# Kernel tuning notes

Hardware: AMD Instinct MI355X
Metric: run time of the kernel (lower is better)

The kernel has to match this reference:

```python
import jax, jax.numpy as jnp
import numpy as np

B, S, D = 32, 2048, 1024
H = 8
D_ATTN = 256
D_HEAD = D_ATTN // H          # 32
D_HEAD_OUT = D // H           # 128
SOFTMAX_TEMP = 1.0


def setup_inputs() -> dict:
    key = jax.random.key(0)
    k0, k1, k2, k3, k4 = jax.random.split(key, 5)
    features = jax.random.normal(k0, (B, S, D), dtype=jnp.float32)
    # truncated-normal(std=0.01) init approximated with scaled normal
    w1 = jax.random.normal(k1, (H, D, D_HEAD), dtype=jnp.float32) * 0.01
    b1 = jax.random.normal(k2, (H, D_HEAD), dtype=jnp.float32) * 0.01
    w2 = jax.random.normal(k3, (H, D_HEAD, D_HEAD_OUT), dtype=jnp.float32) * 0.01
    b2 = jax.random.normal(k4, (H, D_HEAD_OUT), dtype=jnp.float32) * 0.01
    return {"features": features, "w1": w1, "b1": b1, "w2": w2, "b2": b2}


def reference(features, w1, b1, w2, b2):
    Bc, Sc, Dc = features.shape
    # per-head first projection: [B,H,S,d_head]
    h = jnp.einsum('bsd,hde->bhse', features, w1) + b1[None, :, None, :]
    h = jax.nn.gelu(h, approximate=False)  # torch nn.GELU default is exact erf
    # second projection: [B,H,S,d_head_out]
    logits = jnp.einsum('bhse,heo->bhso', h, w2) + b2[None, :, None, :]
    # softmax over seq dim (axis=2)
    smw = jax.nn.softmax(logits / SOFTMAX_TEMP, axis=2)
    # [B,H,S,D/H] -> [B,S,H,D/H] -> [B,S,D]
    smw = smw.transpose(0, 2, 1, 3).reshape(Bc, Sc, Dc)
    return (features * smw).sum(axis=1)  # [B,D]
```

## Files before the change

kernel.cpp:

```cpp
#include <hip/hip_runtime.h>
#include <hip/hip_bf16.h>
#include <math.h>

#define S_  2048
#define D_  1024

typedef __attribute__((ext_vector_type(8))) short short8;
typedef __attribute__((ext_vector_type(4))) float f32x4;

static __device__ __forceinline__ short f2bf(float x) {
    return __builtin_bit_cast(short, __float2bfloat16(x));
}
static __device__ __forceinline__ float bf2f(unsigned short s) {
    unsigned int u = ((unsigned int)s) << 16;
    return __builtin_bit_cast(float, u);
}

__device__ __forceinline__ void gl_lds16(const void* g, void* l) {
    __builtin_amdgcn_global_load_lds(
        (const __attribute__((address_space(1))) unsigned int*)g,
        (__attribute__((address_space(3))) unsigned int*)l, 16, 0, 0);
}

__global__ void prep_w1(const float* __restrict__ w1, short* __restrict__ w1p) {
    int tid = blockIdx.x * 256 + threadIdx.x;
    int lane = tid & 63;
    int fragid = tid >> 6;
    int cf = fragid & 15, ks = fragid >> 4;
    int col = cf * 16 + (lane & 15);
    int h = col >> 5, e = col & 31;
    int d0 = ks * 32 + (lane >> 4) * 8;
    short8 v;
#pragma unroll
    for (int r = 0; r < 8; ++r)
        v[r] = f2bf(w1[((size_t)h * D_ + (d0 + r)) * 32 + e]);
    *(short8*)(w1p + (size_t)tid * 8) = v;
}

__global__ void prep_w2(const float* __restrict__ w2, short* __restrict__ w2p) {
    int tid = blockIdx.x * 256 + threadIdx.x;
    int lane = tid & 63;
    int fragid = tid >> 6;
    int cf2 = fragid & 7, h = fragid >> 3;
    int o = cf2 * 16 + (lane & 15);
    int e0 = (lane >> 4) * 8;
    short8 v;
#pragma unroll
    for (int r = 0; r < 8; ++r)
        v[r] = f2bf(w2[((size_t)h * 32 + (e0 + r)) * 128 + o]);
    *(short8*)(w2p + (size_t)tid * 8) = v;
}

__global__ __launch_bounds__(256) void gemm1(
        const float* __restrict__ feat,
        const short* __restrict__ w1p,
        const float* __restrict__ b1,
        short* __restrict__ hact)
{
    __shared__ short hstage[4][32][136];

    const int tid = threadIdx.x;
    const int wv = tid >> 6;
    const int lane = tid & 63;
    const int lr = lane & 15;
    const int lg = lane >> 4;
    const int wr = wv >> 1, wc = wv & 1;
    const size_t m0 = (size_t)blockIdx.x * 64;

    const float* A0 = feat + (m0 + (size_t)(wr * 32 + lr)) * D_;
    const float* A1 = feat + (m0 + (size_t)(wr * 32 + 16 + lr)) * D_;
    const short8* Bp = (const short8*)w1p;

    const f32x4 vzero = {0.f, 0.f, 0.f, 0.f};
    f32x4 acc[2][8];
#pragma unroll
    for (int i = 0; i < 2; ++i)
#pragma unroll
        for (int j = 0; j < 8; ++j) acc[i][j] = vzero;

    f32x4 p0, p1, p2, p3;
    {
        const int o = lg * 8;
        p0 = *(const f32x4*)(A0 + o); p1 = *(const f32x4*)(A0 + o + 4);
        p2 = *(const f32x4*)(A1 + o); p3 = *(const f32x4*)(A1 + o + 4);
    }

    for (int ks = 0; ks < 32; ++ks) {
        short8 af0, af1;
        af0[0] = f2bf(p0.x); af0[1] = f2bf(p0.y); af0[2] = f2bf(p0.z); af0[3] = f2bf(p0.w);
        af0[4] = f2bf(p1.x); af0[5] = f2bf(p1.y); af0[6] = f2bf(p1.z); af0[7] = f2bf(p1.w);
        af1[0] = f2bf(p2.x); af1[1] = f2bf(p2.y); af1[2] = f2bf(p2.z); af1[3] = f2bf(p2.w);
        af1[4] = f2bf(p3.x); af1[5] = f2bf(p3.y); af1[6] = f2bf(p3.z); af1[7] = f2bf(p3.w);
        if (ks < 31) {
            const int o = (ks + 1) * 32 + lg * 8;
            p0 = *(const f32x4*)(A0 + o); p1 = *(const f32x4*)(A0 + o + 4);
            p2 = *(const f32x4*)(A1 + o); p3 = *(const f32x4*)(A1 + o + 4);
        }
        const short8* Bk = Bp + (size_t)ks * 1024 + (wc * 8) * 64 + lane;
#pragma unroll
        for (int j = 0; j < 8; ++j) {
            short8 b = Bk[j * 64];
            acc[0][j] = __builtin_amdgcn_mfma_f32_16x16x32_bf16(af0, b, acc[0][j], 0, 0, 0);
            acc[1][j] = __builtin_amdgcn_mfma_f32_16x16x32_bf16(af1, b, acc[1][j], 0, 0, 0);
        }
    }

#pragma unroll
    for (int cf = 0; cf < 8; ++cf) {
        const int col = wc * 128 + cf * 16 + lr;
        const float bias = b1[col];
#pragma unroll
        for (int a = 0; a < 2; ++a)
#pragma unroll
        for (int r = 0; r < 4; ++r) {
            const int row = a * 16 + lg * 4 + r;
            float x = acc[a][cf][r] + bias;
            float g = 0.5f * x * (1.0f + erff(x * 0.70710678118654752f));
            hstage[wv][row][cf * 16 + lr] = f2bf(g);
        }
    }
#pragma unroll
    for (int it = 0; it < 8; ++it) {
        const int idx = it * 64 + lane;
        const int row = idx >> 4;
        const int c8 = idx & 15;
        short8 v = *(const short8*)(&hstage[wv][row][c8 * 8]);
        *(short8*)(hact + (m0 + (size_t)(wr * 32 + row)) * 256 + wc * 128 + c8 * 8) = v;
    }
}

__global__ __launch_bounds__(256) void gemm2w(
        const short* __restrict__ hact,
        const float* __restrict__ feat,
        const short* __restrict__ w2p,
        const float* __restrict__ b2,
        float* __restrict__ pnum,
        float* __restrict__ pden)
{
    __shared__ __align__(16) char lds[41216];
    short* hstage = (short*)lds;
    unsigned short* Est = (unsigned short*)(lds + 8192);

    const int tid = threadIdx.x;
    const int wv = tid >> 6;
    const int lane = tid & 63;
    const int lr = lane & 15;
    const int lg = lane >> 4;
    const size_t m0 = (size_t)blockIdx.x * 16;

#pragma unroll
    for (int j = 0; j < 2; ++j)
        gl_lds16(hact + m0 * 256 + (size_t)(j * 256 + tid) * 8,
                 hstage + (j * 256 + wv * 64) * 8);

    float bias2[16];
#pragma unroll
    for (int cf = 0; cf < 16; ++cf)
        bias2[cf] = b2[(2 * wv + (cf >> 3)) * 128 + (cf & 7) * 16 + lr];

    __syncthreads();

    short8 ah0 = *(const short8*)(hstage + lr * 256 + (2 * wv + 0) * 32 + lg * 8);
    short8 ah1 = *(const short8*)(hstage + lr * 256 + (2 * wv + 1) * 32 + lg * 8);
    const f32x4 vzero = {0.f, 0.f, 0.f, 0.f};
#pragma unroll
    for (int cf = 0; cf < 16; ++cf) {
        const int h = 2 * wv + (cf >> 3);
        short8 bw = *(const short8*)(w2p + ((size_t)(h * 8 + (cf & 7)) * 64 + lane) * 8);
        f32x4 c = vzero;
        c = __builtin_amdgcn_mfma_f32_16x16x32_bf16((cf < 8) ? ah0 : ah1, bw, c, 0, 0, 0);
        const int colL = wv * 256 + (cf >> 3) * 128 + (cf & 7) * 16 + lr;
#pragma unroll
        for (int r = 0; r < 4; ++r) {
            float e = __expf(c[r] + bias2[cf]);
            Est[(lg * 4 + r) * 1032 + colL] = (unsigned short)f2bf(e);
        }
    }
    __syncthreads();

    const int c0 = tid * 4;
    f32x4 nacc = vzero, dacc = vzero;
    const float* fb = feat + m0 * D_ + c0;
#pragma unroll
    for (int row = 0; row < 16; ++row) {
        f32x4 fv = *(const f32x4*)(fb + (size_t)row * D_);
        unsigned long long ev = *(const unsigned long long*)(Est + row * 1032 + c0);
        f32x4 e;
        e.x = bf2f((unsigned short)(ev));
        e.y = bf2f((unsigned short)(ev >> 16));
        e.z = bf2f((unsigned short)(ev >> 32));
        e.w = bf2f((unsigned short)(ev >> 48));
        dacc += e;
        nacc += fv * e;
    }
    const size_t pb = (size_t)blockIdx.x * 1024 + c0;
    *(f32x4*)(pnum + pb) = nacc;
    *(f32x4*)(pden + pb) = dacc;
}

__global__ __launch_bounds__(256) void finalize3(
        const float* __restrict__ pnum,
        const float* __restrict__ pden,
        float* __restrict__ out)
{
    const int idx = blockIdx.x * 256 + threadIdx.x;
    const int b = idx >> 10;
    const int d = idx & 1023;
    const size_t base = (size_t)b * 128 * 1024 + d;
    float n = 0.f, dn = 0.f;
    for (int j = 0; j < 128; ++j) {
        n  += pnum[base + (size_t)j * 1024];
        dn += pden[base + (size_t)j * 1024];
    }
    out[idx] = n / dn;
}

extern "C" void kernel_launch(void* const* d_in, const int* in_sizes, int n_in,
                              void* d_out, int out_size, void* d_ws, size_t ws_size,
                              hipStream_t stream) {
    (void)in_sizes; (void)n_in; (void)out_size; (void)ws_size;
    const float* feat = (const float*)d_in[0];
    const float* w1   = (const float*)d_in[1];
    const float* b1   = (const float*)d_in[2];
    const float* w2   = (const float*)d_in[3];
    const float* b2   = (const float*)d_in[4];
    float* out = (float*)d_out;

    char* ws = (char*)d_ws;
    short* hact = (short*)ws;
    float* pnum = (float*)(ws + (32ull << 20));
    float* pden = (float*)(ws + (48ull << 20));
    short* w1p  = (short*)(ws + (64ull << 20));
    short* w2p  = (short*)(ws + (64ull << 20) + (512ull << 10));

    prep_w1<<<128, 256, 0, stream>>>(w1, w1p);
    prep_w2<<<16, 256, 0, stream>>>(w2, w2p);
    gemm1<<<1024, 256, 0, stream>>>(feat, w1p, b1, hact);
    gemm2w<<<4096, 256, 0, stream>>>(hact, feat, w2p, b2, pnum, pden);
    finalize3<<<128, 256, 0, stream>>>(pnum, pden, out);
}
```

Before: 217.2 us.

## Stage gemm1 operands through triple-buffered LDS with async global-to-LDS loads

gemm1 now uses 128-row by 128-column tiles, with each block covering half of the 256 output columns. Feature and packed W1 tiles are loaded straight into a 3-stage LDS ring with global_load_lds, using an XOR swizzle on the A tile to avoid bank conflicts. Previously A came from direct register prefetch and B from per-wave global reads. The goal is to overlap memory latency with MFMA work and let waves share B fragments through LDS. The cost is 72KB of LDS per block, which limits occupancy, and each feature row is now read by two blocks.

```diff
diff --git a/kernel.cpp b/kernel.cpp
--- a/kernel.cpp
+++ b/kernel.cpp
@@ -57,75 +57,125 @@
         const float* __restrict__ b1,
         short* __restrict__ hact)
 {
-    __shared__ short hstage[4][32][136];
+    __shared__ __align__(16) char lds[73728];
+    char* Abuf = lds;
+    char* Bbuf = lds + 49152;
+    short* hstage = (short*)lds;
 
     const int tid = threadIdx.x;
     const int wv = tid >> 6;
     const int lane = tid & 63;
     const int lr = lane & 15;
     const int lg = lane >> 4;
-    const int wr = wv >> 1, wc = wv & 1;
-    const size_t m0 = (size_t)blockIdx.x * 64;
-
-    const float* A0 = feat + (m0 + (size_t)(wr * 32 + lr)) * D_;
-    const float* A1 = feat + (m0 + (size_t)(wr * 32 + 16 + lr)) * D_;
-    const short8* Bp = (const short8*)w1p;
+    const int wr = wv >> 1, wc2 = wv & 1;
+    const int mblk = blockIdx.x >> 1, nblk = blockIdx.x & 1;
+    const size_t m0 = (size_t)mblk * 128;
+
+    const int segA = tid & 7;
+    const int rA = tid >> 3;
+    const int swbA = (segA * 16) ^ ((rA & 7) << 4);
+    const float* gA = feat + (m0 + rA) * D_ + (swbA >> 2);
+    const short* gB = w1p + (size_t)(nblk * 8) * 512 + tid * 8;
+
+    auto stageA = [&](int buf, int ks) {
+        const float* g = gA + ks * 32;
+        char* d = Abuf + buf * 16384 + tid * 16;
+#pragma unroll
+        for (int q = 0; q < 4; ++q)
+            gl_lds16(g + (size_t)q * 32 * D_, d + q * 4096);
+    };
+    auto stageB = [&](int buf, int ks) {
+        const short* g = gB + ks * 8192;
+        char* d = Bbuf + buf * 8192 + tid * 16;
+        gl_lds16(g, d);
+        gl_lds16(g + 2048, d + 4096);
+    };
 
     const f32x4 vzero = {0.f, 0.f, 0.f, 0.f};
-    f32x4 acc[2][8];
-#pragma unroll
-    for (int i = 0; i < 2; ++i)
-#pragma unroll
-        for (int j = 0; j < 8; ++j) acc[i][j] = vzero;
-
-    f32x4 p0, p1, p2, p3;
-    {
-        const int o = lg * 8;
-        p0 = *(const f32x4*)(A0 + o); p1 = *(const f32x4*)(A0 + o + 4);
-        p2 = *(const f32x4*)(A1 + o); p3 = *(const f32x4*)(A1 + o + 4);
-    }
-
-    for (int ks = 0; ks < 32; ++ks) {
-        short8 af0, af1;
-        af0[0] = f2bf(p0.x); af0[1] = f2bf(p0.y); af0[2] = f2bf(p0.z); af0[3] = f2bf(p0.w);
-        af0[4] = f2bf(p1.x); af0[5] = f2bf(p1.y); af0[6] = f2bf(p1.z); af0[7] = f2bf(p1.w);
-        af1[0] = f2bf(p2.x); af1[1] = f2bf(p2.y); af1[2] = f2bf(p2.z); af1[3] = f2bf(p2.w);
-        af1[4] = f2bf(p3.x); af1[5] = f2bf(p3.y); af1[6] = f2bf(p3.z); af1[7] = f2bf(p3.w);
-        if (ks < 31) {
-            const int o = (ks + 1) * 32 + lg * 8;
-            p0 = *(const f32x4*)(A0 + o); p1 = *(const f32x4*)(A0 + o + 4);
-            p2 = *(const f32x4*)(A1 + o); p3 = *(const f32x4*)(A1 + o + 4);
-        }
-        const short8* Bk = Bp + (size_t)ks * 1024 + (wc * 8) * 64 + lane;
-#pragma unroll
-        for (int j = 0; j < 8; ++j) {
-            short8 b = Bk[j * 64];
-            acc[0][j] = __builtin_amdgcn_mfma_f32_16x16x32_bf16(af0, b, acc[0][j], 0, 0, 0);
-            acc[1][j] = __builtin_amdgcn_mfma_f32_16x16x32_bf16(af1, b, acc[1][j], 0, 0, 0);
-        }
-    }
-
-#pragma unroll
-    for (int cf = 0; cf < 8; ++cf) {
-        const int col = wc * 128 + cf * 16 + lr;
-        const float bias = b1[col];
-#pragma unroll
-        for (int a = 0; a < 2; ++a)
-#pragma unroll
-        for (int r = 0; r < 4; ++r) {
-            const int row = a * 16 + lg * 4 + r;
-            float x = acc[a][cf][r] + bias;
-            float g = 0.5f * x * (1.0f + erff(x * 0.70710678118654752f));
-            hstage[wv][row][cf * 16 + lr] = f2bf(g);
-        }
-    }
-#pragma unroll
-    for (int it = 0; it < 8; ++it) {
-        const int idx = it * 64 + lane;
-        const int row = idx >> 4;
-        const int c8 = idx & 15;
-        short8 v = *(const short8*)(&hstage[wv][row][c8 * 8]);
-        *(short8*)(hact + (m0 + (size_t)(wr * 32 + row)) * 256 + wc * 128 + c8 * 8) = v;
+    f32x4 acc[4][4];
+#pragma unroll
+    for (int i = 0; i < 4; ++i)
+#pragma unroll
+        for (int j = 0; j < 4; ++j) acc[i][j] = vzero;
+
+    const int axor = (lr & 7) << 4;
+
+    auto compute = [&](int bi) {
+        const char* Ab = Abuf + bi * 16384;
+        const char* Bb = Bbuf + bi * 8192;
+        short8 bfr0 = *(const short8*)(Bb + ((wc2 * 4 + 0) * 64 + lane) * 16);
+        short8 bfr1 = *(const short8*)(Bb + ((wc2 * 4 + 1) * 64 + lane) * 16);
+        short8 bfr2 = *(const short8*)(Bb + ((wc2 * 4 + 2) * 64 + lane) * 16);
+        short8 bfr3 = *(const short8*)(Bb + ((wc2 * 4 + 3) * 64 + lane) * 16);
+#pragma unroll
+        for (int i = 0; i < 4; ++i) {
+            const int row = wr * 64 + i * 16 + lr;
+            f32x4 alo = *(const f32x4*)(Ab + row * 128 + ((lg * 32) ^ axor));
+            f32x4 ahi = *(const f32x4*)(Ab + row * 128 + ((lg * 32 + 16) ^ axor));
+            short8 af;
+            af[0] = f2bf(alo.x); af[1] = f2bf(alo.y);
+            af[2] = f2bf(alo.z); af[3] = f2bf(alo.w);
+            af[4] = f2bf(ahi.x); af[5] = f2bf(ahi.y);
+            af[6] = f2bf(ahi.z); af[7] = f2bf(ahi.w);
+            acc[i][0] = __builtin_amdgcn_mfma_f32_16x16x32_bf16(af, bfr0, acc[i][0], 0, 0, 0);
+            acc[i][1] = __builtin_amdgcn_mfma_f32_16x16x32_bf16(af, bfr1, acc[i][1], 0, 0, 0);
+            acc[i][2] = __builtin_amdgcn_mfma_f32_16x16x32_bf16(af, bfr2, acc[i][2], 0, 0, 0);
+            acc[i][3] = __builtin_amdgcn_mfma_f32_16x16x32_bf16(af, bfr3, acc[i][3], 0, 0, 0);
+        }
+    };
+
+    stageA(0, 0); stageB(0, 0);
+    stageA(1, 1); stageB(1, 1);
+
+    int cur = 0;
+    for (int ks = 0; ks < 30; ++ks) {
+        asm volatile("s_waitcnt vmcnt(6)" ::: "memory");
+        __builtin_amdgcn_sched_barrier(0);
+        __builtin_amdgcn_s_barrier();
+        int sb = cur + 2; if (sb >= 3) sb -= 3;
+        stageA(sb, ks + 2); stageB(sb, ks + 2);
+        compute(cur);
+        cur = (cur == 2) ? 0 : cur + 1;
+    }
+    asm volatile("s_waitcnt vmcnt(6)" ::: "memory");
+    __builtin_amdgcn_sched_barrier(0);
+    __builtin_amdgcn_s_barrier();
+    compute(cur);
+    cur = (cur == 2) ? 0 : cur + 1;
+    asm volatile("s_waitcnt vmcnt(0)" ::: "memory");
+    __builtin_amdgcn_sched_barrier(0);
+    __builtin_amdgcn_s_barrier();
+    compute(cur);
+    __syncthreads();
+
+#pragma unroll
+    for (int p = 0; p < 2; ++p) {
+        if (wr == p) {
+#pragma unroll
+            for (int j = 0; j < 4; ++j) {
+                const int col = wc2 * 64 + j * 16 + lr;
+                const float bias = b1[nblk * 128 + col];
+#pragma unroll
+                for (int i = 0; i < 4; ++i)
+#pragma unroll
+                for (int r = 0; r < 4; ++r) {
+                    const int lrow = i * 16 + lg * 4 + r;
+                    float x = acc[i][j][r] + bias;
+                    float g = 0.5f * x * (1.0f + erff(x * 0.70710678118654752f));
+                    hstage[lrow * 136 + col] = f2bf(g);
+                }
+            }
+        }
+        __syncthreads();
+#pragma unroll
+        for (int it = 0; it < 4; ++it) {
+            const int idx = it * 256 + tid;
+            const int row = idx >> 4;
+            const int c8 = idx & 15;
+            short8 v = *(const short8*)(hstage + row * 136 + c8 * 8);
+            *(short8*)(hact + (m0 + (size_t)(p * 64 + row)) * 256 + nblk * 128 + c8 * 8) = v;
+        }
+        __syncthreads();
     }
 }
 
```

Result: faster. 187.6 us (-13.6%).
